# Kernel tuning notes

Measured on AMD Instinct MI355X. Metric: run time of the kernel, lower is better.

Reference implementation:

```python
import jax, jax.numpy as jnp
import numpy as np

PI = 3.141592653589793
EPSILON = 1e-3
USE_TANH = True


def setup_inputs() -> dict:
    key = jax.random.key(0)
    k1, k2, k3, k4, k5 = jax.random.split(key, 5)
    b, t, d, p = 4, 8192, 64, 8
    return {
        "query": jax.random.normal(k1, (b, t, d), dtype=jnp.float32),
        "W_Q": jax.random.normal(k2, (p, d), dtype=jnp.float32),
        "W_K": jax.random.normal(k3, (p, d), dtype=jnp.float32),
        "W_V": jax.random.normal(k4, (p, d, d), dtype=jnp.float32),
        "W_O": jax.random.uniform(k5, (p,), dtype=jnp.float32),
    }


def reference(query, W_Q, W_K, W_V, W_O):
    # key = value = query (decoder-only self-attention usage)
    q = jnp.einsum("bti,pi->btp", query, W_Q)
    k = jnp.einsum("bti,pi->btp", query, W_K)
    V = jnp.einsum("bti,pio->btpo", query, W_V)  # (b,t,p,o)
    if USE_TANH:
        q = jnp.tanh(q) * (PI / 4)
        k = jnp.tanh(k) * (PI / 4)
    cos_k = jnp.cos(k)[..., None]  # (b,t,p,1)
    sin_k = jnp.sin(k)[..., None]
    # causal prefix sums over time (axis=-3)
    cos_KV = jnp.cumsum(cos_k * V, axis=-3)
    sin_KV = jnp.cumsum(sin_k * V, axis=-3)
    cos_Q = jnp.cos(q)[..., None]
    sin_Q = jnp.sin(q)[..., None]
    heads = cos_Q * cos_KV + sin_Q * sin_KV  # (b,t,p,o)
    cos_K = jnp.cumsum(cos_k, axis=-3)
    sin_K = jnp.cumsum(sin_k, axis=-3)
    denom = cos_Q * cos_K + sin_Q * sin_K + EPSILON
    heads = heads / denom
    return jnp.einsum("btpo,p->bto", heads, W_O)
```

## Files before the change

### kernel.cpp

```cpp
#include <hip/hip_runtime.h>
#include <hip/hip_bf16.h>
#include <math.h>

#define BB  4
#define TT  8192
#define DD  64
#define PP  8
#define CC  32
#define NCH (TT/CC)
#define QSTR 68
#define TSTR 33

#define EPSV 1e-3f
#define KPI4 0.78539816339744830962f

typedef __attribute__((ext_vector_type(8))) short short8;
typedef __attribute__((ext_vector_type(4))) float f32x4;

__device__ __forceinline__ float bf2f(unsigned short h) {
  return __uint_as_float(((unsigned)h) << 16);
}
__device__ __forceinline__ unsigned short f2bf(float f) {
  unsigned u = __float_as_uint(f);
  u += 0x7fffu + ((u >> 16) & 1u);
  return (unsigned short)(u >> 16);
}
__device__ __forceinline__ float fast_tanh(float x) {
  float e = __expf(2.f * x);
  return 1.f - 2.f * __builtin_amdgcn_rcpf(e + 1.f);
}
__device__ __forceinline__ int zswz(int row, int kb) {
  return (row << 9) + (kb ^ ((row & 7) << 4));
}

__global__ __launch_bounds__(256) void k_pass1(const float* __restrict__ q,
                                               const float* __restrict__ Wk,
                                               const float* __restrict__ Wv,
                                               float* __restrict__ aggC,
                                               float* __restrict__ aggS,
                                               unsigned short* __restrict__ WvTh,
                                               unsigned short* __restrict__ WvTl) {
  const int blk = blockIdx.x;
  const int c = blk & (NCH - 1);
  const int b = blk >> 8;

  __shared__ float SH[64 * QSTR];
  __shared__ float Wks[PP * DD];
  __shared__ float cks[PP * TSTR], sks[PP * TSTR];

  const int tid = threadIdx.x;
  const float* qb = q + ((size_t)b * TT + (size_t)c * CC) * DD;
  for (int g = tid; g < CC * DD; g += 256) SH[(g >> 6) * QSTR + (g & 63)] = qb[g];
  for (int g = tid; g < PP * DD; g += 256) Wks[g] = Wk[g];
  __syncthreads();

  {
    const int t = tid & 31, p = tid >> 5;
    float dk = 0.f;
    const float4* qr = (const float4*)&SH[t * QSTR];
    const float4* wr = (const float4*)&Wks[p * DD];
#pragma unroll
    for (int j = 0; j < 16; ++j) {
      float4 qv = qr[j], wv = wr[j];
      dk = fmaf(qv.x, wv.x, dk); dk = fmaf(qv.y, wv.y, dk);
      dk = fmaf(qv.z, wv.z, dk); dk = fmaf(qv.w, wv.w, dk);
    }
    float ang = fast_tanh(dk) * KPI4;
    float ck = __cosf(ang), sk = __sinf(ang);
    cks[p * TSTR + t] = ck;
    sks[p * TSTR + t] = sk;
    float rc = ck, rs = sk;
#pragma unroll
    for (int d = 16; d >= 1; d >>= 1) {
      rc += __shfl_xor(rc, d, 32);
      rs += __shfl_xor(rs, d, 32);
    }
    if (t == 0) {
      float* s = aggS + ((size_t)(b * PP + p) * NCH + c) * 2;
      s[0] = rc; s[1] = rs;
    }
  }
  __syncthreads();

  {
    const int i = tid & 63, pq = tid >> 6;
    const int p0 = pq, p1 = pq + 4;
    float c0 = 0, s0 = 0, c1 = 0, s1 = 0;
#pragma unroll
    for (int t = 0; t < CC; ++t) {
      float qv = SH[t * QSTR + i];
      c0 = fmaf(cks[p0 * TSTR + t], qv, c0);
      s0 = fmaf(sks[p0 * TSTR + t], qv, s0);
      c1 = fmaf(cks[p1 * TSTR + t], qv, c1);
      s1 = fmaf(sks[p1 * TSTR + t], qv, s1);
    }
    float* a0 = aggC + ((size_t)(b * PP + p0) * NCH + c) * 128;
    float* a1 = aggC + ((size_t)(b * PP + p1) * NCH + c) * 128;
    a0[i] = c0; a0[64 + i] = s0;
    a1[i] = c1; a1[64 + i] = s1;
  }

  if (blk < 8) {
    __syncthreads();
    const int k0 = blk * 64;
    for (int idx = tid; idx < 4096; idx += 256) {
      int kk = idx >> 6, o = idx & 63;
      SH[o * QSTR + kk] = Wv[(size_t)(k0 + kk) * DD + o];
    }
    __syncthreads();
    for (int idx = tid; idx < 4096; idx += 256) {
      int o = idx >> 6, kk = idx & 63;
      float wv = SH[o * QSTR + kk];
      unsigned short hi = f2bf(wv);
      WvTh[(size_t)o * 512 + k0 + kk] = hi;
      WvTl[(size_t)o * 512 + k0 + kk] = f2bf(wv - bf2f(hi));
    }
  }
}

__global__ __launch_bounds__(576) void k_pass2(float* __restrict__ aggC,
                                               float* __restrict__ aggS) {
  const int bp = blockIdx.x;
  const int tid = threadIdx.x;
  __shared__ float totals[4][132];

  const bool act = tid < 520;
  int seg = 0, m = 0;
  float* base = aggC;
  int stride = 128;
  float vals[64];
  if (act) {
    seg = tid / 130;
    m = tid - seg * 130;
    if (m < 128) { base = aggC + (size_t)bp * NCH * 128 + m; stride = 128; }
    else         { base = aggS + (size_t)bp * NCH * 2 + (m - 128); stride = 2; }
    float run = 0.f;
#pragma unroll
    for (int u = 0; u < 64; ++u) vals[u] = base[(size_t)(seg * 64 + u) * stride];
#pragma unroll
    for (int u = 0; u < 64; ++u) run += vals[u];
    totals[seg][m] = run;
  }
  __syncthreads();
  if (act) {
    float r2 = 0.f;
    for (int s = 0; s < seg; ++s) r2 += totals[s][m];
#pragma unroll
    for (int u = 0; u < 64; ++u) {
      float v = vals[u];
      base[(size_t)(seg * 64 + u) * stride] = r2;
      r2 += v;
    }
  }
}

__global__ __launch_bounds__(256, 3) void k_pass3(
    const float* __restrict__ q, const float* __restrict__ Wq,
    const float* __restrict__ Wk, const float* __restrict__ Wo,
    const float* __restrict__ aggC, const float* __restrict__ aggS,
    const unsigned short* __restrict__ WvTh,
    const unsigned short* __restrict__ WvTl,
    float* __restrict__ out) {
  const int blk = blockIdx.x;
  const int c = blk & (NCH - 1);
  const int b = blk >> 8;

  __shared__ float Qs[CC * QSTR];
  __shared__ float Wqs[PP * DD], Wks[PP * DD];
  __shared__ float cqs[PP * TSTR], sqs[PP * TSTR];
  __shared__ float cks[PP * TSTR], sks[PP * TSTR];
  __shared__ float scs[PP * TSTR];
  __shared__ __align__(16) short Zh[CC * 256];
  __shared__ __align__(16) short Zl[CC * 256];

  const int tid = threadIdx.x;
  const int w = tid >> 6, l = tid & 63;
  const int lm = l & 15, lg = l >> 4;
  const int oc = w << 4;

  short8 bhf[8], blf[8];
  {
    const unsigned short* ph_ = WvTh + (size_t)(oc + lm) * 512 + lg * 8;
    const unsigned short* pl_ = WvTl + (size_t)(oc + lm) * 512 + lg * 8;
#pragma unroll
    for (int kk = 0; kk < 8; ++kk) {
      bhf[kk] = *(const short8*)(ph_ + kk * 32);
      blf[kk] = *(const short8*)(pl_ + kk * 32);
    }
  }

  const float* qb = q + ((size_t)b * TT + (size_t)c * CC) * DD;
  for (int g = tid; g < CC * DD; g += 256) Qs[(g >> 6) * QSTR + (g & 63)] = qb[g];
  for (int g = tid; g < PP * DD; g += 256) { Wqs[g] = Wq[g]; Wks[g] = Wk[g]; }
  __syncthreads();

  {
    const int t = tid & 31, p = tid >> 5;
    float dq = 0.f, dk = 0.f;
    const float4* qr  = (const float4*)&Qs[t * QSTR];
    const float4* wqr = (const float4*)&Wqs[p * DD];
    const float4* wkr = (const float4*)&Wks[p * DD];
#pragma unroll
    for (int j = 0; j < 16; ++j) {
      float4 qv = qr[j], w0 = wqr[j], w1 = wkr[j];
      dq = fmaf(qv.x, w0.x, dq); dq = fmaf(qv.y, w0.y, dq);
      dq = fmaf(qv.z, w0.z, dq); dq = fmaf(qv.w, w0.w, dq);
      dk = fmaf(qv.x, w1.x, dk); dk = fmaf(qv.y, w1.y, dk);
      dk = fmaf(qv.z, w1.z, dk); dk = fmaf(qv.w, w1.w, dk);
    }
    float ang = fast_tanh(dq) * KPI4;
    float cq = __cosf(ang), sq = __sinf(ang);
    ang = fast_tanh(dk) * KPI4;
    float ck = __cosf(ang), sk = __sinf(ang);
    cqs[p * TSTR + t] = cq; sqs[p * TSTR + t] = sq;
    cks[p * TSTR + t] = ck; sks[p * TSTR + t] = sk;
    float rc = ck, rs = sk;
#pragma unroll
    for (int d = 1; d < 32; d <<= 1) {
      float tc = __shfl_up(rc, (unsigned)d, 32);
      float ts = __shfl_up(rs, (unsigned)d, 32);
      if (t >= d) { rc += tc; rs += ts; }
    }
    const float* sgl = aggS + ((size_t)(b * PP + p) * NCH + c) * 2;
    rc += sgl[0]; rs += sgl[1];
    float den = fmaf(cq, rc, fmaf(sq, rs, EPSV));
    scs[p * TSTR + t] = Wo[p] * __builtin_amdgcn_rcpf(den);
  }
  __syncthreads();

  f32x4 acc0 = {0, 0, 0, 0}, acc1 = {0, 0, 0, 0};

#pragma unroll
  for (int h = 0; h < 2; ++h) {
    {
      const int p = h * 4 + w;
      const float* prC = aggC + ((size_t)(b * PP + p) * NCH + c) * 128;
      float Ac = prC[l], As = prC[64 + l];
      const int kb = (w * 64 + l) * 2;
#pragma unroll 8
      for (int t = 0; t < CC; ++t) {
        float qv = Qs[t * QSTR + l];
        Ac = fmaf(cks[p * TSTR + t], qv, Ac);
        As = fmaf(sks[p * TSTR + t], qv, As);
        float z = scs[p * TSTR + t] * fmaf(cqs[p * TSTR + t], Ac, sqs[p * TSTR + t] * As);
        unsigned u = __float_as_uint(z);
        unsigned r = u + 0x7fffu + ((u >> 16) & 1u);
        int zb = zswz(t, kb);
        ((unsigned short*)Zh)[zb >> 1] = (unsigned short)(r >> 16);
        float lo = z - __uint_as_float(r & 0xffff0000u);
        ((unsigned short*)Zl)[zb >> 1] = (unsigned short)(__float_as_uint(lo) >> 16);
      }
    }
    __syncthreads();
#pragma unroll
    for (int kk = 0; kk < 8; ++kk) {
      const int rb0 = zswz(lm, kk * 64 + lg * 16);
      const int rb1 = zswz(16 + lm, kk * 64 + lg * 16);
      short8 ah0 = *(const short8*)((const char*)Zh + rb0);
      short8 al0 = *(const short8*)((const char*)Zl + rb0);
      short8 ah1 = *(const short8*)((const char*)Zh + rb1);
      short8 al1 = *(const short8*)((const char*)Zl + rb1);
      acc0 = __builtin_amdgcn_mfma_f32_16x16x32_bf16(ah0, bhf[kk], acc0, 0, 0, 0);
      acc1 = __builtin_amdgcn_mfma_f32_16x16x32_bf16(ah1, bhf[kk], acc1, 0, 0, 0);
      acc0 = __builtin_amdgcn_mfma_f32_16x16x32_bf16(al0, bhf[kk], acc0, 0, 0, 0);
      acc1 = __builtin_amdgcn_mfma_f32_16x16x32_bf16(al1, bhf[kk], acc1, 0, 0, 0);
      acc0 = __builtin_amdgcn_mfma_f32_16x16x32_bf16(ah0, blf[kk], acc0, 0, 0, 0);
      acc1 = __builtin_amdgcn_mfma_f32_16x16x32_bf16(ah1, blf[kk], acc1, 0, 0, 0);
    }
    if (h == 0) {
      const unsigned short* ph_ = WvTh + (size_t)(oc + lm) * 512 + 256 + lg * 8;
      const unsigned short* pl_ = WvTl + (size_t)(oc + lm) * 512 + 256 + lg * 8;
#pragma unroll
      for (int kk = 0; kk < 8; ++kk) {
        bhf[kk] = *(const short8*)(ph_ + kk * 32);
        blf[kk] = *(const short8*)(pl_ + kk * 32);
      }
    }
    __syncthreads();
  }

  {
    float* ob = out + ((size_t)b * TT + (size_t)c * CC + lg * 4) * DD + oc + lm;
#pragma unroll
    for (int r = 0; r < 4; ++r) {
      ob[r * DD] = acc0[r];
      ob[(16 + r) * DD] = acc1[r];
    }
  }
}

extern "C" void kernel_launch(void* const* d_in, const int* in_sizes, int n_in,
                              void* d_out, int out_size, void* d_ws, size_t ws_size,
                              hipStream_t stream) {
  const float* q  = (const float*)d_in[0];
  const float* Wq = (const float*)d_in[1];
  const float* Wk = (const float*)d_in[2];
  const float* Wv = (const float*)d_in[3];
  const float* Wo = (const float*)d_in[4];
  float* out = (float*)d_out;

  float* aggC = (float*)d_ws;
  float* aggS = aggC + (size_t)BB * PP * NCH * 128;
  unsigned short* WvTh = (unsigned short*)(aggS + (size_t)BB * PP * NCH * 2);
  unsigned short* WvTl = WvTh + (size_t)512 * 64;

  k_pass1<<<BB * NCH, 256, 0, stream>>>(q, Wk, Wv, aggC, aggS, WvTh, WvTl);
  k_pass2<<<BB * PP, 576, 0, stream>>>(aggC, aggS);
  k_pass3<<<BB * NCH, 256, 0, stream>>>(q, Wq, Wk, Wo, aggC, aggS, WvTh, WvTl, out);
}
```

Baseline: 48.75 us.

## Replace LDS coefficient tables with readlane broadcasts and shrink shared memory

Per-(p,t) cos/sin and scale coefficients now stay in registers and are broadcast with readlane, so the separate LDS tables and their loads go away. In both passes the q·W dot products read directly from global memory instead of staged LDS copies. The q column is cached in registers, and pass3's shared footprint is cut so occupancy can rise to 4 blocks per SIMD group. The trade-off is higher register pressure under the tighter launch bound, with a risk of spills, plus extra global reads for the dot products.

```diff
diff --git a/kernel.cpp b/kernel.cpp
--- a/kernel.cpp
+++ b/kernel.cpp
@@ -8,8 +8,7 @@
 #define PP  8
 #define CC  32
 #define NCH (TT/CC)
-#define QSTR 68
-#define TSTR 33
+#define SSTR 65
 
 #define EPSV 1e-3f
 #define KPI4 0.78539816339744830962f
@@ -29,8 +28,8 @@
   float e = __expf(2.f * x);
   return 1.f - 2.f * __builtin_amdgcn_rcpf(e + 1.f);
 }
-__device__ __forceinline__ int zswz(int row, int kb) {
-  return (row << 9) + (kb ^ ((row & 7) << 4));
+__device__ __forceinline__ float rlane(float v, int lane) {
+  return __uint_as_float(__builtin_amdgcn_readlane(__float_as_uint(v), lane));
 }
 
 __global__ __launch_bounds__(256) void k_pass1(const float* __restrict__ q,
@@ -44,21 +43,21 @@
   const int c = blk & (NCH - 1);
   const int b = blk >> 8;
 
-  __shared__ float SH[64 * QSTR];
-  __shared__ float Wks[PP * DD];
-  __shared__ float cks[PP * TSTR], sks[PP * TSTR];
+  __shared__ float SH[64 * SSTR];
 
   const int tid = threadIdx.x;
+  const int w = tid >> 6, l = tid & 63;
+  const int sub = l >> 5, tA = l & 31;
+  const int pA = w + 4 * sub;
+
   const float* qb = q + ((size_t)b * TT + (size_t)c * CC) * DD;
-  for (int g = tid; g < CC * DD; g += 256) SH[(g >> 6) * QSTR + (g & 63)] = qb[g];
-  for (int g = tid; g < PP * DD; g += 256) Wks[g] = Wk[g];
-  __syncthreads();
-
-  {
-    const int t = tid & 31, p = tid >> 5;
+  for (int g = tid; g < CC * DD; g += 256) SH[(g >> 6) * SSTR + (g & 63)] = qb[g];
+
+  float ckR, skR;
+  {
+    const float4* qr = (const float4*)(qb + tA * DD);
+    const float4* wr = (const float4*)(Wk + pA * DD);
     float dk = 0.f;
-    const float4* qr = (const float4*)&SH[t * QSTR];
-    const float4* wr = (const float4*)&Wks[p * DD];
 #pragma unroll
     for (int j = 0; j < 16; ++j) {
       float4 qv = qr[j], wv = wr[j];
@@ -66,38 +65,36 @@
       dk = fmaf(qv.z, wv.z, dk); dk = fmaf(qv.w, wv.w, dk);
     }
     float ang = fast_tanh(dk) * KPI4;
-    float ck = __cosf(ang), sk = __sinf(ang);
-    cks[p * TSTR + t] = ck;
-    sks[p * TSTR + t] = sk;
-    float rc = ck, rs = sk;
+    ckR = __cosf(ang); skR = __sinf(ang);
+    float rc = ckR, rs = skR;
 #pragma unroll
     for (int d = 16; d >= 1; d >>= 1) {
       rc += __shfl_xor(rc, d, 32);
       rs += __shfl_xor(rs, d, 32);
     }
-    if (t == 0) {
-      float* s = aggS + ((size_t)(b * PP + p) * NCH + c) * 2;
-      s[0] = rc; s[1] = rs;
-    }
-  }
-  __syncthreads();
-
-  {
-    const int i = tid & 63, pq = tid >> 6;
-    const int p0 = pq, p1 = pq + 4;
+    if (tA == 0) {
+      float* s = aggS + ((size_t)(b * PP + pA) * NCH + c) * 2;
+      *(float2*)s = make_float2(rc, rs);
+    }
+  }
+  __syncthreads();
+
+  {
+    float qcol[CC];
+#pragma unroll
+    for (int t = 0; t < CC; ++t) qcol[t] = SH[t * SSTR + l];
     float c0 = 0, s0 = 0, c1 = 0, s1 = 0;
 #pragma unroll
     for (int t = 0; t < CC; ++t) {
-      float qv = SH[t * QSTR + i];
-      c0 = fmaf(cks[p0 * TSTR + t], qv, c0);
-      s0 = fmaf(sks[p0 * TSTR + t], qv, s0);
-      c1 = fmaf(cks[p1 * TSTR + t], qv, c1);
-      s1 = fmaf(sks[p1 * TSTR + t], qv, s1);
-    }
-    float* a0 = aggC + ((size_t)(b * PP + p0) * NCH + c) * 128;
-    float* a1 = aggC + ((size_t)(b * PP + p1) * NCH + c) * 128;
-    a0[i] = c0; a0[64 + i] = s0;
-    a1[i] = c1; a1[64 + i] = s1;
+      float a0 = rlane(ckR, t), b0 = rlane(skR, t);
+      float a1 = rlane(ckR, t + 32), b1 = rlane(skR, t + 32);
+      c0 = fmaf(a0, qcol[t], c0); s0 = fmaf(b0, qcol[t], s0);
+      c1 = fmaf(a1, qcol[t], c1); s1 = fmaf(b1, qcol[t], s1);
+    }
+    float* a0p = aggC + ((size_t)(b * PP + w) * NCH + c) * 128;
+    float* a1p = aggC + ((size_t)(b * PP + w + 4) * NCH + c) * 128;
+    a0p[l] = c0; a0p[64 + l] = s0;
+    a1p[l] = c1; a1p[64 + l] = s1;
   }
 
   if (blk < 8) {
@@ -105,12 +102,12 @@
     const int k0 = blk * 64;
     for (int idx = tid; idx < 4096; idx += 256) {
       int kk = idx >> 6, o = idx & 63;
-      SH[o * QSTR + kk] = Wv[(size_t)(k0 + kk) * DD + o];
+      SH[o * SSTR + kk] = Wv[(size_t)(k0 + kk) * DD + o];
     }
     __syncthreads();
     for (int idx = tid; idx < 4096; idx += 256) {
       int o = idx >> 6, kk = idx & 63;
-      float wv = SH[o * QSTR + kk];
+      float wv = SH[o * SSTR + kk];
       unsigned short hi = f2bf(wv);
       WvTh[(size_t)o * 512 + k0 + kk] = hi;
       WvTl[(size_t)o * 512 + k0 + kk] = f2bf(wv - bf2f(hi));
@@ -154,7 +151,7 @@
   }
 }
 
-__global__ __launch_bounds__(256, 3) void k_pass3(
+__global__ __launch_bounds__(256, 4) void k_pass3(
     const float* __restrict__ q, const float* __restrict__ Wq,
     const float* __restrict__ Wk, const float* __restrict__ Wo,
     const float* __restrict__ aggC, const float* __restrict__ aggS,
@@ -165,18 +162,15 @@
   const int c = blk & (NCH - 1);
   const int b = blk >> 8;
 
-  __shared__ float Qs[CC * QSTR];
-  __shared__ float Wqs[PP * DD], Wks[PP * DD];
-  __shared__ float cqs[PP * TSTR], sqs[PP * TSTR];
-  __shared__ float cks[PP * TSTR], sks[PP * TSTR];
-  __shared__ float scs[PP * TSTR];
-  __shared__ __align__(16) short Zh[CC * 256];
-  __shared__ __align__(16) short Zl[CC * 256];
+  __shared__ float Qs[CC * 64];
+  __shared__ __align__(16) short Zbuf[2 * CC * 256];
 
   const int tid = threadIdx.x;
   const int w = tid >> 6, l = tid & 63;
   const int lm = l & 15, lg = l >> 4;
   const int oc = w << 4;
+  const int sub = l >> 5, tA = l & 31;
+  const int pA = w + 4 * sub;
 
   short8 bhf[8], blf[8];
   {
@@ -190,16 +184,14 @@
   }
 
   const float* qb = q + ((size_t)b * TT + (size_t)c * CC) * DD;
-  for (int g = tid; g < CC * DD; g += 256) Qs[(g >> 6) * QSTR + (g & 63)] = qb[g];
-  for (int g = tid; g < PP * DD; g += 256) { Wqs[g] = Wq[g]; Wks[g] = Wk[g]; }
-  __syncthreads();
-
-  {
-    const int t = tid & 31, p = tid >> 5;
+  for (int g = tid; g < CC * DD; g += 256) Qs[g] = qb[g];
+
+  float ckR, skR, alR, beR;
+  {
+    const float4* qr  = (const float4*)(qb + tA * DD);
+    const float4* wqr = (const float4*)(Wq + pA * DD);
+    const float4* wkr = (const float4*)(Wk + pA * DD);
     float dq = 0.f, dk = 0.f;
-    const float4* qr  = (const float4*)&Qs[t * QSTR];
-    const float4* wqr = (const float4*)&Wqs[p * DD];
-    const float4* wkr = (const float4*)&Wks[p * DD];
 #pragma unroll
     for (int j = 0; j < 16; ++j) {
       float4 qv = qr[j], w0 = wqr[j], w1 = wkr[j];
@@ -211,55 +203,50 @@
     float ang = fast_tanh(dq) * KPI4;
     float cq = __cosf(ang), sq = __sinf(ang);
     ang = fast_tanh(dk) * KPI4;
-    float ck = __cosf(ang), sk = __sinf(ang);
-    cqs[p * TSTR + t] = cq; sqs[p * TSTR + t] = sq;
-    cks[p * TSTR + t] = ck; sks[p * TSTR + t] = sk;
-    float rc = ck, rs = sk;
+    ckR = __cosf(ang); skR = __sinf(ang);
+    float rc = ckR, rs = skR;
 #pragma unroll
     for (int d = 1; d < 32; d <<= 1) {
       float tc = __shfl_up(rc, (unsigned)d, 32);
       float ts = __shfl_up(rs, (unsigned)d, 32);
-      if (t >= d) { rc += tc; rs += ts; }
-    }
-    const float* sgl = aggS + ((size_t)(b * PP + p) * NCH + c) * 2;
-    rc += sgl[0]; rs += sgl[1];
+      if (tA >= d) { rc += tc; rs += ts; }
+    }
+    const float2 sgl = *(const float2*)(aggS + ((size_t)(b * PP + pA) * NCH + c) * 2);
+    rc += sgl.x; rs += sgl.y;
     float den = fmaf(cq, rc, fmaf(sq, rs, EPSV));
-    scs[p * TSTR + t] = Wo[p] * __builtin_amdgcn_rcpf(den);
-  }
-  __syncthreads();
-
+    float ws = Wo[pA] * __builtin_amdgcn_rcpf(den);
+    alR = ws * cq; beR = ws * sq;
+  }
+
+  const float* prC0 = aggC + ((size_t)(b * PP + w) * NCH + c) * 128;
+  const float* prC1 = aggC + ((size_t)(b * PP + w + 4) * NCH + c) * 128;
+  float Ac0 = prC0[l], As0 = prC0[64 + l];
+  float Ac1 = prC1[l], As1 = prC1[64 + l];
+
+  __syncthreads();
+
+  float qcol[CC];
+#pragma unroll
+  for (int t = 0; t < CC; ++t) qcol[t] = Qs[t * 64 + l];
+
+  const int kb = (w << 7) + (l << 1);
+  int xad[8];
+#pragma unroll
+  for (int r = 0; r < 8; ++r) xad[r] = kb ^ (r << 4);
+
+  char* zbase = (char*)Zbuf;
   f32x4 acc0 = {0, 0, 0, 0}, acc1 = {0, 0, 0, 0};
 
-#pragma unroll
-  for (int h = 0; h < 2; ++h) {
-    {
-      const int p = h * 4 + w;
-      const float* prC = aggC + ((size_t)(b * PP + p) * NCH + c) * 128;
-      float Ac = prC[l], As = prC[64 + l];
-      const int kb = (w * 64 + l) * 2;
-#pragma unroll 8
-      for (int t = 0; t < CC; ++t) {
-        float qv = Qs[t * QSTR + l];
-        Ac = fmaf(cks[p * TSTR + t], qv, Ac);
-        As = fmaf(sks[p * TSTR + t], qv, As);
-        float z = scs[p * TSTR + t] * fmaf(cqs[p * TSTR + t], Ac, sqs[p * TSTR + t] * As);
-        unsigned u = __float_as_uint(z);
-        unsigned r = u + 0x7fffu + ((u >> 16) & 1u);
-        int zb = zswz(t, kb);
-        ((unsigned short*)Zh)[zb >> 1] = (unsigned short)(r >> 16);
-        float lo = z - __uint_as_float(r & 0xffff0000u);
-        ((unsigned short*)Zl)[zb >> 1] = (unsigned short)(__float_as_uint(lo) >> 16);
-      }
-    }
-    __syncthreads();
+  auto phaseC = [&]() {
 #pragma unroll
     for (int kk = 0; kk < 8; ++kk) {
-      const int rb0 = zswz(lm, kk * 64 + lg * 16);
-      const int rb1 = zswz(16 + lm, kk * 64 + lg * 16);
-      short8 ah0 = *(const short8*)((const char*)Zh + rb0);
-      short8 al0 = *(const short8*)((const char*)Zl + rb0);
-      short8 ah1 = *(const short8*)((const char*)Zh + rb1);
-      short8 al1 = *(const short8*)((const char*)Zl + rb1);
+      const int sw = (kk * 64 + lg * 16) ^ ((lm & 7) << 4);
+      const int rb0 = (lm << 9) + sw;
+      const int rb1 = ((16 + lm) << 9) + sw;
+      short8 ah0 = *(const short8*)(zbase + rb0);
+      short8 al0 = *(const short8*)(zbase + 16384 + rb0);
+      short8 ah1 = *(const short8*)(zbase + rb1);
+      short8 al1 = *(const short8*)(zbase + 16384 + rb1);
       acc0 = __builtin_amdgcn_mfma_f32_16x16x32_bf16(ah0, bhf[kk], acc0, 0, 0, 0);
       acc1 = __builtin_amdgcn_mfma_f32_16x16x32_bf16(ah1, bhf[kk], acc1, 0, 0, 0);
       acc0 = __builtin_amdgcn_mfma_f32_16x16x32_bf16(al0, bhf[kk], acc0, 0, 0, 0);
@@ -267,17 +254,49 @@
       acc0 = __builtin_amdgcn_mfma_f32_16x16x32_bf16(ah0, blf[kk], acc0, 0, 0, 0);
       acc1 = __builtin_amdgcn_mfma_f32_16x16x32_bf16(ah1, blf[kk], acc1, 0, 0, 0);
     }
-    if (h == 0) {
-      const unsigned short* ph_ = WvTh + (size_t)(oc + lm) * 512 + 256 + lg * 8;
-      const unsigned short* pl_ = WvTl + (size_t)(oc + lm) * 512 + 256 + lg * 8;
-#pragma unroll
-      for (int kk = 0; kk < 8; ++kk) {
-        bhf[kk] = *(const short8*)(ph_ + kk * 32);
-        blf[kk] = *(const short8*)(pl_ + kk * 32);
-      }
-    }
-    __syncthreads();
-  }
+  };
+
+#pragma unroll
+  for (int t = 0; t < CC; ++t) {
+    float ck = rlane(ckR, t), sk = rlane(skR, t);
+    float al = rlane(alR, t), be = rlane(beR, t);
+    Ac0 = fmaf(ck, qcol[t], Ac0);
+    As0 = fmaf(sk, qcol[t], As0);
+    float z = fmaf(al, Ac0, be * As0);
+    unsigned u = __float_as_uint(z);
+    unsigned r = u + 0x7fffu + ((u >> 16) & 1u);
+    float lo = z - __uint_as_float(r & 0xffff0000u);
+    *(short*)(zbase + (t << 9) + xad[t & 7]) = (short)(r >> 16);
+    *(short*)(zbase + 16384 + (t << 9) + xad[t & 7]) = (short)(__float_as_uint(lo) >> 16);
+  }
+  __syncthreads();
+  phaseC();
+  {
+    const unsigned short* ph_ = WvTh + (size_t)(oc + lm) * 512 + 256 + lg * 8;
+    const unsigned short* pl_ = WvTl + (size_t)(oc + lm) * 512 + 256 + lg * 8;
+#pragma unroll
+    for (int kk = 0; kk < 8; ++kk) {
+      bhf[kk] = *(const short8*)(ph_ + kk * 32);
+      blf[kk] = *(const short8*)(pl_ + kk * 32);
+    }
+  }
+  __syncthreads();
+
+#pragma unroll
+  for (int t = 0; t < CC; ++t) {
+    float ck = rlane(ckR, t + 32), sk = rlane(skR, t + 32);
+    float al = rlane(alR, t + 32), be = rlane(beR, t + 32);
+    Ac1 = fmaf(ck, qcol[t], Ac1);
+    As1 = fmaf(sk, qcol[t], As1);
+    float z = fmaf(al, Ac1, be * As1);
+    unsigned u = __float_as_uint(z);
+    unsigned r = u + 0x7fffu + ((u >> 16) & 1u);
+    float lo = z - __uint_as_float(r & 0xffff0000u);
+    *(short*)(zbase + (t << 9) + xad[t & 7]) = (short)(r >> 16);
+    *(short*)(zbase + 16384 + (t << 9) + xad[t & 7]) = (short)(__float_as_uint(lo) >> 16);
+  }
+  __syncthreads();
+  phaseC();
 
   {
     float* ob = out + ((size_t)b * TT + (size_t)c * CC + lg * 4) * DD + oc + lm;
```

Measured after the change: 66.17 us. 35.7% more time.

## Interleave chunk aggregates into one strided buffer and spread Wv conversion across blocks

Applied to the files above, without the earlier changes.

Merges the separate aggC (128 floats per chunk) and aggS (2 floats per chunk) buffers into one 130-float-stride record. The pass2 scan then uses a single uniform strided access instead of branching between two layouts. Pass1 now computes the per-chunk cos/sin sums with a serial loop over shared memory instead of a warp shuffle reduction. The Wv split-bf16 transpose is spread across 64 blocks of 8 rows each instead of 8 blocks of 64 rows, shortening the tail on those blocks. The 130-float stride breaks the alignment of the per-chunk records.

```diff
diff --git a/kernel.cpp b/kernel.cpp
--- a/kernel.cpp
+++ b/kernel.cpp
@@ -8,6 +8,7 @@
 #define PP  8
 #define CC  32
 #define NCH (TT/CC)
+#define AGG_STRIDE 130
 #define QSTR 68
 #define TSTR 33
 
@@ -36,8 +37,7 @@
 __global__ __launch_bounds__(256) void k_pass1(const float* __restrict__ q,
                                                const float* __restrict__ Wk,
                                                const float* __restrict__ Wv,
-                                               float* __restrict__ aggC,
-                                               float* __restrict__ aggS,
+                                               float* __restrict__ agg,
                                                unsigned short* __restrict__ WvTh,
                                                unsigned short* __restrict__ WvTl) {
   const int blk = blockIdx.x;
@@ -66,19 +66,8 @@
       dk = fmaf(qv.z, wv.z, dk); dk = fmaf(qv.w, wv.w, dk);
     }
     float ang = fast_tanh(dk) * KPI4;
-    float ck = __cosf(ang), sk = __sinf(ang);
-    cks[p * TSTR + t] = ck;
-    sks[p * TSTR + t] = sk;
-    float rc = ck, rs = sk;
-#pragma unroll
-    for (int d = 16; d >= 1; d >>= 1) {
-      rc += __shfl_xor(rc, d, 32);
-      rs += __shfl_xor(rs, d, 32);
-    }
-    if (t == 0) {
-      float* s = aggS + ((size_t)(b * PP + p) * NCH + c) * 2;
-      s[0] = rc; s[1] = rs;
-    }
+    cks[p * TSTR + t] = __cosf(ang);
+    sks[p * TSTR + t] = __sinf(ang);
   }
   __syncthreads();
 
@@ -94,22 +83,37 @@
       c1 = fmaf(cks[p1 * TSTR + t], qv, c1);
       s1 = fmaf(sks[p1 * TSTR + t], qv, s1);
     }
-    float* a0 = aggC + ((size_t)(b * PP + p0) * NCH + c) * 128;
-    float* a1 = aggC + ((size_t)(b * PP + p1) * NCH + c) * 128;
+    float* a0 = agg + (size_t)((b * PP + p0) * NCH + c) * AGG_STRIDE;
+    float* a1 = agg + (size_t)((b * PP + p1) * NCH + c) * AGG_STRIDE;
     a0[i] = c0; a0[64 + i] = s0;
     a1[i] = c1; a1[64 + i] = s1;
   }
-
-  if (blk < 8) {
+  if (tid < 16) {
+    const int p = tid & 7;
+    float s2 = 0.f;
+    if (tid < 8) {
+      for (int t = 0; t < CC; ++t) s2 += cks[p * TSTR + t];
+      agg[(size_t)((b * PP + p) * NCH + c) * AGG_STRIDE + 128] = s2;
+    } else {
+      for (int t = 0; t < CC; ++t) s2 += sks[p * TSTR + t];
+      agg[(size_t)((b * PP + p) * NCH + c) * AGG_STRIDE + 129] = s2;
+    }
+  }
+
+  if (blk < 64) {
     __syncthreads();
-    const int k0 = blk * 64;
-    for (int idx = tid; idx < 4096; idx += 256) {
+    const int k0 = blk * 8;
+#pragma unroll
+    for (int r = 0; r < 2; ++r) {
+      int idx = tid + r * 256;
       int kk = idx >> 6, o = idx & 63;
       SH[o * QSTR + kk] = Wv[(size_t)(k0 + kk) * DD + o];
     }
     __syncthreads();
-    for (int idx = tid; idx < 4096; idx += 256) {
-      int o = idx >> 6, kk = idx & 63;
+#pragma unroll
+    for (int r = 0; r < 2; ++r) {
+      int idx = tid + r * 256;
+      int o = idx >> 3, kk = idx & 7;
       float wv = SH[o * QSTR + kk];
       unsigned short hi = f2bf(wv);
       WvTh[(size_t)o * 512 + k0 + kk] = hi;
@@ -118,25 +122,22 @@
   }
 }
 
-__global__ __launch_bounds__(576) void k_pass2(float* __restrict__ aggC,
-                                               float* __restrict__ aggS) {
+__global__ __launch_bounds__(576) void k_pass2(float* __restrict__ agg) {
   const int bp = blockIdx.x;
   const int tid = threadIdx.x;
   __shared__ float totals[4][132];
 
   const bool act = tid < 520;
   int seg = 0, m = 0;
-  float* base = aggC;
-  int stride = 128;
+  float* base = agg;
   float vals[64];
   if (act) {
     seg = tid / 130;
     m = tid - seg * 130;
-    if (m < 128) { base = aggC + (size_t)bp * NCH * 128 + m; stride = 128; }
-    else         { base = aggS + (size_t)bp * NCH * 2 + (m - 128); stride = 2; }
+    base = agg + (size_t)bp * NCH * AGG_STRIDE + m;
     float run = 0.f;
 #pragma unroll
-    for (int u = 0; u < 64; ++u) vals[u] = base[(size_t)(seg * 64 + u) * stride];
+    for (int u = 0; u < 64; ++u) vals[u] = base[(size_t)(seg * 64 + u) * AGG_STRIDE];
 #pragma unroll
     for (int u = 0; u < 64; ++u) run += vals[u];
     totals[seg][m] = run;
@@ -148,7 +149,7 @@
 #pragma unroll
     for (int u = 0; u < 64; ++u) {
       float v = vals[u];
-      base[(size_t)(seg * 64 + u) * stride] = r2;
+      base[(size_t)(seg * 64 + u) * AGG_STRIDE] = r2;
       r2 += v;
     }
   }
@@ -157,7 +158,7 @@
 __global__ __launch_bounds__(256, 3) void k_pass3(
     const float* __restrict__ q, const float* __restrict__ Wq,
     const float* __restrict__ Wk, const float* __restrict__ Wo,
-    const float* __restrict__ aggC, const float* __restrict__ aggS,
+    const float* __restrict__ pref,
     const unsigned short* __restrict__ WvTh,
     const unsigned short* __restrict__ WvTl,
     float* __restrict__ out) {
@@ -210,10 +211,11 @@
     }
     float ang = fast_tanh(dq) * KPI4;
     float cq = __cosf(ang), sq = __sinf(ang);
+    cqs[p * TSTR + t] = cq; sqs[p * TSTR + t] = sq;
     ang = fast_tanh(dk) * KPI4;
     float ck = __cosf(ang), sk = __sinf(ang);
-    cqs[p * TSTR + t] = cq; sqs[p * TSTR + t] = sq;
     cks[p * TSTR + t] = ck; sks[p * TSTR + t] = sk;
+
     float rc = ck, rs = sk;
 #pragma unroll
     for (int d = 1; d < 32; d <<= 1) {
@@ -221,20 +223,22 @@
       float ts = __shfl_up(rs, (unsigned)d, 32);
       if (t >= d) { rc += tc; rs += ts; }
     }
-    const float* sgl = aggS + ((size_t)(b * PP + p) * NCH + c) * 2;
-    rc += sgl[0]; rs += sgl[1];
+    const float* pr = pref + (size_t)((b * PP + p) * NCH + c) * AGG_STRIDE;
+    rc += pr[128]; rs += pr[129];
     float den = fmaf(cq, rc, fmaf(sq, rs, EPSV));
     scs[p * TSTR + t] = Wo[p] * __builtin_amdgcn_rcpf(den);
   }
   __syncthreads();
 
+  char* zbaseH = (char*)Zh;
+  char* zbaseL = (char*)Zl;
   f32x4 acc0 = {0, 0, 0, 0}, acc1 = {0, 0, 0, 0};
 
 #pragma unroll
   for (int h = 0; h < 2; ++h) {
     {
       const int p = h * 4 + w;
-      const float* prC = aggC + ((size_t)(b * PP + p) * NCH + c) * 128;
+      const float* prC = pref + (size_t)((b * PP + p) * NCH + c) * AGG_STRIDE;
       float Ac = prC[l], As = prC[64 + l];
       const int kb = (w * 64 + l) * 2;
 #pragma unroll 8
@@ -246,9 +250,9 @@
         unsigned u = __float_as_uint(z);
         unsigned r = u + 0x7fffu + ((u >> 16) & 1u);
         int zb = zswz(t, kb);
-        ((unsigned short*)Zh)[zb >> 1] = (unsigned short)(r >> 16);
+        *(short*)(zbaseH + zb) = (short)(r >> 16);
         float lo = z - __uint_as_float(r & 0xffff0000u);
-        ((unsigned short*)Zl)[zb >> 1] = (unsigned short)(__float_as_uint(lo) >> 16);
+        *(short*)(zbaseL + zb) = (short)(__float_as_uint(lo) >> 16);
       }
     }
     __syncthreads();
@@ -256,10 +260,10 @@
     for (int kk = 0; kk < 8; ++kk) {
       const int rb0 = zswz(lm, kk * 64 + lg * 16);
       const int rb1 = zswz(16 + lm, kk * 64 + lg * 16);
-      short8 ah0 = *(const short8*)((const char*)Zh + rb0);
-      short8 al0 = *(const short8*)((const char*)Zl + rb0);
-      short8 ah1 = *(const short8*)((const char*)Zh + rb1);
-      short8 al1 = *(const short8*)((const char*)Zl + rb1);
+      short8 ah0 = *(const short8*)(zbaseH + rb0);
+      short8 al0 = *(const short8*)(zbaseL + rb0);
+      short8 ah1 = *(const short8*)(zbaseH + rb1);
+      short8 al1 = *(const short8*)(zbaseL + rb1);
       acc0 = __builtin_amdgcn_mfma_f32_16x16x32_bf16(ah0, bhf[kk], acc0, 0, 0, 0);
       acc1 = __builtin_amdgcn_mfma_f32_16x16x32_bf16(ah1, bhf[kk], acc1, 0, 0, 0);
       acc0 = __builtin_amdgcn_mfma_f32_16x16x32_bf16(al0, bhf[kk], acc0, 0, 0, 0);
@@ -298,13 +302,11 @@
   const float* Wv = (const float*)d_in[3];
   const float* Wo = (const float*)d_in[4];
   float* out = (float*)d_out;
-
-  float* aggC = (float*)d_ws;
-  float* aggS = aggC + (size_t)BB * PP * NCH * 128;
-  unsigned short* WvTh = (unsigned short*)(aggS + (size_t)BB * PP * NCH * 2);
+  float* agg = (float*)d_ws;
+  unsigned short* WvTh = (unsigned short*)(agg + (size_t)BB * PP * NCH * AGG_STRIDE);
   unsigned short* WvTl = WvTh + (size_t)512 * 64;
 
-  k_pass1<<<BB * NCH, 256, 0, stream>>>(q, Wk, Wv, aggC, aggS, WvTh, WvTl);
-  k_pass2<<<BB * PP, 576, 0, stream>>>(aggC, aggS);
-  k_pass3<<<BB * NCH, 256, 0, stream>>>(q, Wq, Wk, Wo, aggC, aggS, WvTh, WvTl, out);
-}
+  k_pass1<<<BB * NCH, 256, 0, stream>>>(q, Wk, Wv, agg, WvTh, WvTl);
+  k_pass2<<<BB * PP, 576, 0, stream>>>(agg);
+  k_pass3<<<BB * NCH, 256, 0, stream>>>(q, Wq, Wk, Wo, agg, WvTh, WvTl, out);
+}
```

New measurement: 47.33 us. -2.9%, faster.
